# Performance work log

Hardware: AMD Instinct MI355X
Metric: run time of the kernel (lower is better)

The kernel has to match this reference:

```python
import jax, jax.numpy as jnp
import numpy as np

N_HEADS = 32
N_KV = 8
N_REP = N_HEADS // N_KV  # 4
HD = 128
ROPE_THETA = 500000.0


def _rope_tables(seq_len, hd, theta):
    inv = 1.0 / (theta ** (np.arange(0, hd, 2, dtype=np.float32) / hd))  # [hd/2]
    t = np.arange(seq_len, dtype=np.float32)
    ang = np.outer(t, inv)  # [T, hd/2]
    return jnp.asarray(np.cos(ang)), jnp.asarray(np.sin(ang))


def setup_inputs() -> dict:
    key = jax.random.key(0)
    ks = jax.random.split(key, 8)
    B, T, D = 2, 2048, 4096
    s = 0.02
    x = jax.random.normal(ks[0], (B, T, D), jnp.float32)
    wq = jax.random.normal(ks[1], (D, D), jnp.float32) * s
    wk = jax.random.normal(ks[2], (N_KV * HD, D), jnp.float32) * s
    wv = jax.random.normal(ks[3], (N_KV * HD, D), jnp.float32) * s
    wo = jax.random.normal(ks[4], (D, D), jnp.float32) * s
    cache_k = jnp.zeros((B, T, N_KV, HD), jnp.float32)
    cache_v = jnp.zeros((B, T, N_KV, HD), jnp.float32)
    cos, sin = _rope_tables(T, HD, ROPE_THETA)
    mask = jnp.zeros((1,), jnp.float32)  # accepted by forward but never applied
    return {"x": x, "wq": wq, "wk": wk, "wv": wv, "wo": wo,
            "cache_k": cache_k, "cache_v": cache_v,
            "cos": cos, "sin": sin, "mask": mask, "start_pos": 0}


def _apply_rope(t, cos, sin):
    # t: [B, T, H, HD]; pairs (t0,t1) along last dim act as complex numbers
    tr = t.reshape(*t.shape[:-1], HD // 2, 2)
    re, im = tr[..., 0], tr[..., 1]
    c = cos[None, :, None, :]  # [1,T,1,HD/2]
    s = sin[None, :, None, :]
    out = jnp.stack([re * c - im * s, re * s + im * c], axis=-1)
    return out.reshape(t.shape)


def reference(x, wq, wk, wv, wo, cache_k, cache_v, cos, sin, mask, start_pos):
    B, T, D = x.shape
    q = (x @ wq.T).reshape(B, T, N_HEADS, HD)
    k = (x @ wk.T).reshape(B, T, N_KV, HD)
    v = (x @ wv.T).reshape(B, T, N_KV, HD)

    q = _apply_rope(q, cos, sin)
    k = _apply_rope(k, cos, sin)

    # KV-cache write (start_pos is a python int)
    cache_k = cache_k.at[:, start_pos:start_pos + T].set(k)
    cache_v = cache_v.at[:, start_pos:start_pos + T].set(v)
    keys = cache_k[:, :start_pos + T]   # [B,S,Kv,HD]
    vals = cache_v[:, :start_pos + T]

    # GQA attention without materializing repeat_kv: q head h uses kv head h // N_REP
    q5 = q.reshape(B, T, N_KV, N_REP, HD)
    scale = 1.0 / jnp.sqrt(jnp.float32(HD))
    scores = jnp.einsum('btkrd,bskd->bkrts', q5, keys) * scale  # [B,Kv,Rep,T,S]
    # NOTE: source forward never adds `mask` to scores; faithfully omitted.
    probs = jax.nn.softmax(scores, axis=-1)
    ctx = jnp.einsum('bkrts,bskd->btkrd', probs, vals)  # [B,T,Kv,Rep,HD]
    cat = ctx.reshape(B, T, N_HEADS * HD)
    return cat @ wo.T
```

## Files before the change

kernel.cpp:

```cpp
#include <hip/hip_runtime.h>
#include <hip/hip_bf16.h>
#include <stdint.h>


typedef short bf16x8 __attribute__((ext_vector_type(8)));
typedef float f32x4  __attribute__((ext_vector_type(4)));

#define GLB_AS(p) ((__attribute__((address_space(1))) void*)(p))
#define LDS_AS(p) ((__attribute__((address_space(3))) void*)(p))

__device__ __forceinline__ float bf2f(ushort u) {
    union { unsigned int i; float f; } v; v.i = ((unsigned int)u) << 16; return v.f;
}
__device__ __forceinline__ ushort f2bf(float f) {
    union { float f; unsigned int i; } v; v.f = f;
    unsigned int r = v.i + 0x7FFFu + ((v.i >> 16) & 1u);
    return (ushort)(r >> 16);
}
__device__ __forceinline__ unsigned int pk_bf16(float a, float b) {
    return (unsigned int)f2bf(a) | ((unsigned int)f2bf(b) << 16);
}
__device__ __forceinline__ unsigned int cvtpk2(float lo, float hi) {
    unsigned int r;
    asm("v_cvt_pk_bf16_f32 %0, %1, %2" : "=v"(r) : "v"(lo), "v"(hi));
    return r;
}
__device__ __forceinline__ void store_c(ushort* p, float v) { *p = f2bf(v); }
__device__ __forceinline__ void store_c(float*  p, float v) { *p = v; }

__global__ __launch_bounds__(256) void cast_f2b(
    const float4* __restrict__ src, ushort4* __restrict__ dst, int n4)
{
    int i = blockIdx.x * 256 + threadIdx.x;
    if (i < n4) {
        float4 v = src[i];
        ushort4 o;
        o.x = f2bf(v.x); o.y = f2bf(v.y); o.z = f2bf(v.z); o.w = f2bf(v.w);
        dst[i] = o;
    }
}

template <typename OT>
__global__ __launch_bounds__(256) void gemm_nt(
    const ushort* __restrict__ A, const ushort* __restrict__ B,
    OT* __restrict__ C, int M, int N, int K)
{
    __shared__ __align__(16) ushort lA[128 * 32];
    __shared__ __align__(16) ushort lB[128 * 32];

    const int tid  = threadIdx.x;
    const int lane = tid & 63;
    const int w    = tid >> 6;
    const int wm   = w >> 1, wn = w & 1;
    const int quad = lane >> 4, l16 = lane & 15;
    const int bm   = blockIdx.y * 128, bn = blockIdx.x * 128;

    f32x4 acc[4][4];
#pragma unroll
    for (int i = 0; i < 4; i++)
#pragma unroll
        for (int j = 0; j < 4; j++) acc[i][j] = (f32x4){0.f, 0.f, 0.f, 0.f};

    const ushort* pa0 = A + (size_t)(bm + (tid >> 2)) * K + (tid & 3) * 8;
    const ushort* pb0 = B + (size_t)(bn + (tid >> 2)) * K + (tid & 3) * 8;
    char* ldsA0 = (char*)lA + (tid & 192) * 16;
    char* ldsA1 = ldsA0 + 4096;
    char* ldsB0 = (char*)lB + (tid & 192) * 16;
    char* ldsB1 = ldsB0 + 4096;
    const size_t rowskip = (size_t)64 * K;

    for (int k0 = 0; k0 < K; k0 += 32) {
        __builtin_amdgcn_global_load_lds(GLB_AS(pa0 + k0),           LDS_AS(ldsA0), 16, 0, 0);
        __builtin_amdgcn_global_load_lds(GLB_AS(pa0 + rowskip + k0), LDS_AS(ldsA1), 16, 0, 0);
        __builtin_amdgcn_global_load_lds(GLB_AS(pb0 + k0),           LDS_AS(ldsB0), 16, 0, 0);
        __builtin_amdgcn_global_load_lds(GLB_AS(pb0 + rowskip + k0), LDS_AS(ldsB1), 16, 0, 0);
        __syncthreads();

        bf16x8 a[4], b[4];
#pragma unroll
        for (int i = 0; i < 4; i++)
            a[i] = *(const bf16x8*)&lA[(wm * 64 + i * 16 + l16) * 32 + quad * 8];
#pragma unroll
        for (int j = 0; j < 4; j++)
            b[j] = *(const bf16x8*)&lB[(wn * 64 + j * 16 + l16) * 32 + quad * 8];
#pragma unroll
        for (int i = 0; i < 4; i++)
#pragma unroll
            for (int j = 0; j < 4; j++)
                acc[i][j] = __builtin_amdgcn_mfma_f32_16x16x32_bf16(a[i], b[j], acc[i][j], 0, 0, 0);
        __syncthreads();
    }

#pragma unroll
    for (int i = 0; i < 4; i++)
#pragma unroll
        for (int j = 0; j < 4; j++)
#pragma unroll
            for (int r = 0; r < 4; r++) {
                int row = bm + wm * 64 + i * 16 + quad * 4 + r;
                int col = bn + wn * 64 + j * 16 + l16;
                store_c(&C[(size_t)row * N + col], acc[i][j][r]);
            }
}

__global__ __launch_bounds__(256) void rope_kernel(
    ushort* __restrict__ X, const float* __restrict__ cosv,
    const float* __restrict__ sinv, int ldx, int tprs, float scale)
{
    int gid = blockIdx.x * 256 + threadIdx.x;
    int m  = gid >> tprs;
    int pi = (gid & ((1 << tprs) - 1)) * 4;
    int t  = m & 2047;
    int i  = pi & 63;
    float4 c4 = *(const float4*)&cosv[t * 64 + i];
    float4 s4 = *(const float4*)&sinv[t * 64 + i];
    ushort* px = X + (size_t)m * ldx + pi * 2;
    uint4 d = *(const uint4*)px;
    unsigned int parts[4] = {d.x, d.y, d.z, d.w};
    float cc[4] = {c4.x, c4.y, c4.z, c4.w};
    float ss[4] = {s4.x, s4.y, s4.z, s4.w};
#pragma unroll
    for (int p = 0; p < 4; p++) {
        float re = bf2f((ushort)(parts[p] & 0xffffu));
        float im = bf2f((ushort)(parts[p] >> 16));
        float re2 = (re * cc[p] - im * ss[p]) * scale;
        float im2 = (re * ss[p] + im * cc[p]) * scale;
        parts[p] = pk_bf16(re2, im2);
    }
    *(uint4*)px = make_uint4(parts[0], parts[1], parts[2], parts[3]);
}

__global__ __launch_bounds__(256) void transpose_v(
    const ushort* __restrict__ KV, ushort* __restrict__ Vt)
{
    __shared__ ushort tile[32][33];
    int n0 = blockIdx.x * 32, m0 = blockIdx.y * 32;
    int tx = threadIdx.x & 31, ty = threadIdx.x >> 5;
#pragma unroll
    for (int r = ty; r < 32; r += 8)
        tile[r][tx] = KV[(size_t)(m0 + r) * 2048 + 1024 + n0 + tx];
    __syncthreads();
    int b  = m0 >> 11;
    int t0 = m0 & 2047;
#pragma unroll
    for (int r = ty; r < 32; r += 8)
        Vt[(size_t)b * 2097152 + (size_t)(n0 + r) * 2048 + t0 + tx] = tile[tx][r];
}

__global__ __launch_bounds__(512) void flash_attn(
    const ushort* __restrict__ Q, const ushort* __restrict__ KV,
    const ushort* __restrict__ Vt, ushort* __restrict__ ctx)
{
    __shared__ __align__(16) ushort lK[64 * 128];
    __shared__ __align__(16) ushort lV[128 * 64];
    __shared__ __align__(16) ushort lP[8 * 16 * 72];

    const int qt = blockIdx.x, h = blockIdx.y, b = blockIdx.z;
    const int kv = h >> 2;
    const int tid = threadIdx.x, lane = tid & 63, w = tid >> 6;
    const int quad = lane >> 4, l16 = lane & 15;

    const int q0 = qt * 128 + w * 16;
    const size_t qrow = (size_t)(b * 2048 + q0 + l16) * 4096 + h * 128;
    bf16x8 bQ[4];
#pragma unroll
    for (int ks = 0; ks < 4; ks++)
        bQ[ks] = *(const bf16x8*)&Q[qrow + ks * 32 + quad * 8];

    f32x4 o[8];
#pragma unroll
    for (int dc = 0; dc < 8; dc++) o[dc] = (f32x4){0.f, 0.f, 0.f, 0.f};
    float m = -1e30f, l = 0.f;

    const ushort* gK = KV + (size_t)(b * 2048) * 2048 + kv * 128;
    const ushort* gV = Vt + (size_t)(b * 8 + kv) * 2048 * 128;
    ushort* pw = &lP[w * 16 * 72];

    const int keyb = tid >> 4, dsub = tid & 15;
    const int db   = tid >> 3, ssub = tid & 7;
    const ushort* baseK = gK + (size_t)keyb * 2048 + (dsub ^ (keyb & 15)) * 8;
    const ushort* baseV = gV + (size_t)db * 2048 + (ssub ^ (db & 7)) * 8;
    char* ldsK = (char*)lK + (tid & 448) * 16;
    char* ldsV = (char*)lV + (tid & 448) * 16;

    for (int s0 = 0; s0 < 2048; s0 += 64) {
#pragma unroll
        for (int rep = 0; rep < 2; rep++) {
            __builtin_amdgcn_global_load_lds(
                GLB_AS(baseK + (size_t)(s0 + rep * 32) * 2048),
                LDS_AS(ldsK + rep * 8192), 16, 0, 0);
            __builtin_amdgcn_global_load_lds(
                GLB_AS(baseV + (size_t)rep * 131072 + s0),
                LDS_AS(ldsV + rep * 8192), 16, 0, 0);
        }
        __syncthreads();

        f32x4 scT[4];
#pragma unroll
        for (int g = 0; g < 4; g++) scT[g] = (f32x4){0.f, 0.f, 0.f, 0.f};
#pragma unroll
        for (int g = 0; g < 4; g++)
#pragma unroll
            for (int ks = 0; ks < 4; ks++) {
                bf16x8 aK = *(const bf16x8*)&lK[(g * 16 + l16) * 128 + ((ks * 4 + quad) ^ l16) * 8];
                scT[g] = __builtin_amdgcn_mfma_f32_16x16x32_bf16(aK, bQ[ks], scT[g], 0, 0, 0);
            }

        float tmax = scT[0][0];
#pragma unroll
        for (int g = 0; g < 4; g++)
#pragma unroll
            for (int r = 0; r < 4; r++) tmax = fmaxf(tmax, scT[g][r]);
        tmax = fmaxf(tmax, __shfl_xor(tmax, 16, 64));
        tmax = fmaxf(tmax, __shfl_xor(tmax, 32, 64));

        if (__any(tmax > m + 8.f)) {
            float mnew = fmaxf(m, tmax);
            float alpha = exp2f(m - mnew);
            m = mnew;
            l *= alpha;
#pragma unroll
            for (int dc = 0; dc < 8; dc++)
#pragma unroll
                for (int r = 0; r < 4; r++) o[dc][r] *= alpha;
        }

        float p[16];
        float ts = 0.f;
#pragma unroll
        for (int i = 0; i < 16; i++) {
            p[i] = exp2f(scT[i >> 2][i & 3] - m);
            ts += p[i];
        }
        ts += __shfl_xor(ts, 16, 64);
        ts += __shfl_xor(ts, 32, 64);
        l += ts;

#pragma unroll
        for (int g = 0; g < 4; g++) {
            uint2 pk;
            pk.x = cvtpk2(p[g * 4 + 0], p[g * 4 + 1]);
            pk.y = cvtpk2(p[g * 4 + 2], p[g * 4 + 3]);
            *(uint2*)&pw[l16 * 72 + g * 16 + quad * 4] = pk;
        }
        bf16x8 bP[2];
#pragma unroll
        for (int c = 0; c < 2; c++)
            bP[c] = *(const bf16x8*)&pw[l16 * 72 + c * 32 + quad * 8];

#pragma unroll
        for (int dc = 0; dc < 8; dc++)
#pragma unroll
            for (int c = 0; c < 2; c++) {
                bf16x8 aV = *(const bf16x8*)&lV[(dc * 16 + l16) * 64 + ((c * 4 + quad) ^ (l16 & 7)) * 8];
                o[dc] = __builtin_amdgcn_mfma_f32_16x16x32_bf16(aV, bP[c], o[dc], 0, 0, 0);
            }
        __syncthreads();
    }

    float inv = 1.0f / l;
#pragma unroll
    for (int dc = 0; dc < 8; dc++) {
        uint2 pk;
        pk.x = cvtpk2(o[dc][0] * inv, o[dc][1] * inv);
        pk.y = cvtpk2(o[dc][2] * inv, o[dc][3] * inv);
        *(uint2*)&ctx[qrow + dc * 16 + quad * 4] = pk;
    }
}

extern "C" void kernel_launch(void* const* d_in, const int* in_sizes, int n_in,
                              void* d_out, int out_size, void* d_ws, size_t ws_size,
                              hipStream_t stream)
{
    const float* x    = (const float*)d_in[0];
    const float* wq   = (const float*)d_in[1];
    const float* wk   = (const float*)d_in[2];
    const float* wv   = (const float*)d_in[3];
    const float* wo   = (const float*)d_in[4];
    const float* cosv = (const float*)d_in[7];
    const float* sinv = (const float*)d_in[8];
    float* out = (float*)d_out;

    ushort* Xb   = (ushort*)d_ws;
    ushort* ctx  = Xb;
    ushort* Wbig = Xb   + (size_t)16 * 1024 * 1024;
    ushort* Wsm  = Wbig + (size_t)16 * 1024 * 1024;
    ushort* Vt   = Wsm;
    ushort* Q    = Wsm  + (size_t)8  * 1024 * 1024;
    ushort* KV   = Q    + (size_t)16 * 1024 * 1024;

    dim3 blk(256);
    cast_f2b<<<16384, blk, 0, stream>>>((const float4*)x,  (ushort4*)Xb,   4194304);
    cast_f2b<<<16384, blk, 0, stream>>>((const float4*)wq, (ushort4*)Wbig, 4194304);
    cast_f2b<<<4096,  blk, 0, stream>>>((const float4*)wk, (ushort4*)Wsm,  1048576);
    cast_f2b<<<4096,  blk, 0, stream>>>((const float4*)wv, (ushort4*)(Wsm + (size_t)4194304), 1048576);

    gemm_nt<<<dim3(32, 32), blk, 0, stream>>>(Xb, Wbig, Q,  4096, 4096, 4096);
    gemm_nt<<<dim3(16, 32), blk, 0, stream>>>(Xb, Wsm,  KV, 4096, 2048, 4096);

    cast_f2b<<<16384, blk, 0, stream>>>((const float4*)wo, (ushort4*)Wbig, 4194304);

    rope_kernel<<<8192, blk, 0, stream>>>(Q,  cosv, sinv, 4096, 9,
                                          0.08838834764831845f * 1.4426950408889634f);
    rope_kernel<<<2048, blk, 0, stream>>>(KV, cosv, sinv, 2048, 7, 1.0f);
    transpose_v<<<dim3(32, 128), blk, 0, stream>>>(KV, Vt);

    flash_attn<<<dim3(16, 32, 2), dim3(512), 0, stream>>>(Q, KV, Vt, ctx);

    gemm_nt<<<dim3(32, 32), blk, 0, stream>>>(ctx, Wbig, out, 4096, 4096, 4096);
}
```

Baseline: 963.4 us.

## Replace 128x128 GEMM with 256x256 double-buffered swizzled 8-wave GEMM

```diff
diff --git a/kernel.cpp b/kernel.cpp
--- a/kernel.cpp
+++ b/kernel.cpp
@@ -27,6 +27,12 @@
 }
 __device__ __forceinline__ void store_c(ushort* p, float v) { *p = f2bf(v); }
 __device__ __forceinline__ void store_c(float*  p, float v) { *p = v; }
+
+__device__ __forceinline__ void barr() {
+    asm volatile("" ::: "memory");
+    __builtin_amdgcn_s_barrier();
+    asm volatile("" ::: "memory");
+}
 
 __global__ __launch_bounds__(256) void cast_f2b(
     const float4* __restrict__ src, ushort4* __restrict__ dst, int n4)
@@ -40,67 +46,154 @@
     }
 }
 
+enum { OFF_A0 = 0, OFF_A1 = 16384, OFF_B0 = 32768, OFF_B1 = 49152, BUFSZ = 65536 };
+
+__device__ __forceinline__ void rdA(const char* half, bf16x8 (&a)[4][2],
+                                    int wm, int quad, int l16) {
+    const int cx = l16 & 7;
+#pragma unroll
+    for (int m2 = 0; m2 < 4; m2++)
+#pragma unroll
+        for (int ks = 0; ks < 2; ks++)
+            a[m2][ks] = *(const bf16x8*)(half + (wm * 64 + m2 * 16 + l16) * 128
+                                              + (((ks * 4 + quad) ^ cx) * 16));
+}
+__device__ __forceinline__ void rdB(const char* half, bf16x8 (&b)[2][2],
+                                    int wn, int quad, int l16) {
+    const int cx = l16 & 7;
+#pragma unroll
+    for (int n2 = 0; n2 < 2; n2++)
+#pragma unroll
+        for (int ks = 0; ks < 2; ks++)
+            b[n2][ks] = *(const bf16x8*)(half + (wn * 32 + n2 * 16 + l16) * 128
+                                              + (((ks * 4 + quad) ^ cx) * 16));
+}
+template <int MH, int NH>
+__device__ __forceinline__ void mmq(f32x4 (&acc)[2][2][4][2],
+                                    const bf16x8 (&a)[4][2], const bf16x8 (&b)[2][2]) {
+    __builtin_amdgcn_s_setprio(1);
+#pragma unroll
+    for (int m2 = 0; m2 < 4; m2++)
+#pragma unroll
+        for (int n2 = 0; n2 < 2; n2++)
+#pragma unroll
+            for (int ks = 0; ks < 2; ks++)
+                acc[MH][NH][m2][n2] = __builtin_amdgcn_mfma_f32_16x16x32_bf16(
+                    a[m2][ks], b[n2][ks], acc[MH][NH][m2][n2], 0, 0, 0);
+    __builtin_amdgcn_s_setprio(0);
+}
+__device__ __forceinline__ void stage_half(const char* src, char* dst, size_t kb) {
+    __builtin_amdgcn_global_load_lds(GLB_AS(src),           LDS_AS(dst),        16, 0, 0);
+    __builtin_amdgcn_global_load_lds(GLB_AS(src + 64 * kb), LDS_AS(dst + 8192), 16, 0, 0);
+}
+
+#define GATE8 asm volatile("s_waitcnt vmcnt(8)" ::: "memory")
+#define GATE0 asm volatile("s_waitcnt vmcnt(0)" ::: "memory")
+#define GATEN ((void)0)
+
+#define DO_TILE(LBUF, KO, DO_STAGE, GATE)                                        \
+    {                                                                            \
+        const char* Lb = lds + (LBUF) * BUFSZ;                                   \
+        char* Sb = ldsW + (LBUF) * BUFSZ;                                        \
+                                                         \
+        rdA(Lb + OFF_A0, a, wm, quad, l16);                                      \
+        rdB(Lb + OFF_B0, b0, wn, quad, l16);                                     \
+        barr();                                                                  \
+        mmq<0, 0>(acc, a, b0);                                                   \
+        barr();                                                                  \
+                                       \
+        rdB(Lb + OFF_B1, b1, wn, quad, l16);                                     \
+        if (DO_STAGE) {                                                          \
+            stage_half(aSrc + (KO), Sb + OFF_A0, kb);                            \
+            stage_half(bSrc + (KO), Sb + OFF_B0, kb);                            \
+        }                                                                        \
+        barr();                                                                  \
+        mmq<0, 1>(acc, a, b1);                                                   \
+        barr();                                                                  \
+                      \
+        rdA(Lb + OFF_A1, a, wm, quad, l16);                                      \
+        if (DO_STAGE) stage_half(bSrc + 128 * kb + (KO), Sb + OFF_B1, kb);       \
+        barr();                                                                  \
+        mmq<1, 1>(acc, a, b1);                                                   \
+        barr();                                                                  \
+                             \
+        if (DO_STAGE) stage_half(aSrc + 128 * kb + (KO), Sb + OFF_A1, kb);       \
+        barr();                                                                  \
+        mmq<1, 0>(acc, a, b0);                                                   \
+        GATE;                                                                    \
+        barr();                                                                  \
+    }
+
 template <typename OT>
-__global__ __launch_bounds__(256) void gemm_nt(
+__global__ __launch_bounds__(512, 2) void gemm_nt256(
     const ushort* __restrict__ A, const ushort* __restrict__ B,
-    OT* __restrict__ C, int M, int N, int K)
-{
-    __shared__ __align__(16) ushort lA[128 * 32];
-    __shared__ __align__(16) ushort lB[128 * 32];
-
-    const int tid  = threadIdx.x;
-    const int lane = tid & 63;
-    const int w    = tid >> 6;
-    const int wm   = w >> 1, wn = w & 1;
+    OT* __restrict__ C, int N, int K)
+{
+    __shared__ __align__(16) char lds[131072];
+
+    const int tid = threadIdx.x, lane = tid & 63, w = tid >> 6;
+    const int wm = w >> 2, wn = w & 3;
     const int quad = lane >> 4, l16 = lane & 15;
-    const int bm   = blockIdx.y * 128, bn = blockIdx.x * 128;
-
-    f32x4 acc[4][4];
-#pragma unroll
-    for (int i = 0; i < 4; i++)
-#pragma unroll
-        for (int j = 0; j < 4; j++) acc[i][j] = (f32x4){0.f, 0.f, 0.f, 0.f};
-
-    const ushort* pa0 = A + (size_t)(bm + (tid >> 2)) * K + (tid & 3) * 8;
-    const ushort* pb0 = B + (size_t)(bn + (tid >> 2)) * K + (tid & 3) * 8;
-    char* ldsA0 = (char*)lA + (tid & 192) * 16;
-    char* ldsA1 = ldsA0 + 4096;
-    char* ldsB0 = (char*)lB + (tid & 192) * 16;
-    char* ldsB1 = ldsB0 + 4096;
-    const size_t rowskip = (size_t)64 * K;
-
-    for (int k0 = 0; k0 < K; k0 += 32) {
-        __builtin_amdgcn_global_load_lds(GLB_AS(pa0 + k0),           LDS_AS(ldsA0), 16, 0, 0);
-        __builtin_amdgcn_global_load_lds(GLB_AS(pa0 + rowskip + k0), LDS_AS(ldsA1), 16, 0, 0);
-        __builtin_amdgcn_global_load_lds(GLB_AS(pb0 + k0),           LDS_AS(ldsB0), 16, 0, 0);
-        __builtin_amdgcn_global_load_lds(GLB_AS(pb0 + rowskip + k0), LDS_AS(ldsB1), 16, 0, 0);
-        __syncthreads();
-
-        bf16x8 a[4], b[4];
-#pragma unroll
-        for (int i = 0; i < 4; i++)
-            a[i] = *(const bf16x8*)&lA[(wm * 64 + i * 16 + l16) * 32 + quad * 8];
-#pragma unroll
-        for (int j = 0; j < 4; j++)
-            b[j] = *(const bf16x8*)&lB[(wn * 64 + j * 16 + l16) * 32 + quad * 8];
-#pragma unroll
-        for (int i = 0; i < 4; i++)
-#pragma unroll
-            for (int j = 0; j < 4; j++)
-                acc[i][j] = __builtin_amdgcn_mfma_f32_16x16x32_bf16(a[i], b[j], acc[i][j], 0, 0, 0);
-        __syncthreads();
-    }
-
-#pragma unroll
-    for (int i = 0; i < 4; i++)
-#pragma unroll
-        for (int j = 0; j < 4; j++)
-#pragma unroll
-            for (int r = 0; r < 4; r++) {
-                int row = bm + wm * 64 + i * 16 + quad * 4 + r;
-                int col = bn + wn * 64 + j * 16 + l16;
-                store_c(&C[(size_t)row * N + col], acc[i][j][r]);
-            }
+
+    const int nwg = gridDim.x;
+    const int swz = ((int)blockIdx.x & 7) * (nwg >> 3) + ((int)blockIdx.x >> 3);
+    const int nx  = N >> 8;
+    const int bm  = (swz / nx) * 256, bn = (swz % nx) * 256;
+
+    const size_t kb = (size_t)K * 2;
+
+    const int srow = tid >> 3;
+    const int gch  = (tid & 7) ^ (srow & 7);
+    const char* aSrc = (const char*)A + (size_t)(bm + srow) * kb + gch * 16;
+    const char* bSrc = (const char*)B + (size_t)(bn + srow) * kb + gch * 16;
+    char* ldsW = lds + w * 1024;
+
+    f32x4 acc[2][2][4][2];
+#pragma unroll
+    for (int i = 0; i < 2; i++)
+#pragma unroll
+        for (int j = 0; j < 2; j++)
+#pragma unroll
+            for (int m2 = 0; m2 < 4; m2++)
+#pragma unroll
+                for (int n2 = 0; n2 < 2; n2++)
+                    acc[i][j][m2][n2] = (f32x4){0.f, 0.f, 0.f, 0.f};
+
+    bf16x8 a[4][2], b0[2][2], b1[2][2];
+
+    stage_half(aSrc,                ldsW + OFF_A0, kb);
+    stage_half(aSrc + 128 * kb,     ldsW + OFF_A1, kb);
+    stage_half(bSrc,                ldsW + OFF_B0, kb);
+    stage_half(bSrc + 128 * kb,     ldsW + OFF_B1, kb);
+    stage_half(aSrc + 128,            ldsW + BUFSZ + OFF_A0, kb);
+    stage_half(aSrc + 128 * kb + 128, ldsW + BUFSZ + OFF_A1, kb);
+    stage_half(bSrc + 128,            ldsW + BUFSZ + OFF_B0, kb);
+    stage_half(bSrc + 128 * kb + 128, ldsW + BUFSZ + OFF_B1, kb);
+    GATE8;
+    barr();
+
+    int ko = 256;
+    for (int it = 0; it < 31; ++it, ko += 256) {
+        DO_TILE(0, ko,       true, GATE8);
+        DO_TILE(1, ko + 128, true, GATE8);
+    }
+    DO_TILE(0, 0, false, GATE0);
+    DO_TILE(1, 0, false, GATEN);
+
+#pragma unroll
+    for (int MH = 0; MH < 2; MH++)
+#pragma unroll
+        for (int NH = 0; NH < 2; NH++)
+#pragma unroll
+            for (int m2 = 0; m2 < 4; m2++)
+#pragma unroll
+                for (int n2 = 0; n2 < 2; n2++)
+#pragma unroll
+                    for (int r = 0; r < 4; r++) {
+                        int row = bm + MH * 128 + wm * 64 + m2 * 16 + quad * 4 + r;
+                        int col = bn + NH * 128 + wn * 32 + n2 * 16 + l16;
+                        store_c(&C[(size_t)row * N + col], acc[MH][NH][m2][n2][r]);
+                    }
 }
 
 __global__ __launch_bounds__(256) void rope_kernel(
@@ -295,8 +388,8 @@
     cast_f2b<<<4096,  blk, 0, stream>>>((const float4*)wk, (ushort4*)Wsm,  1048576);
     cast_f2b<<<4096,  blk, 0, stream>>>((const float4*)wv, (ushort4*)(Wsm + (size_t)4194304), 1048576);
 
-    gemm_nt<<<dim3(32, 32), blk, 0, stream>>>(Xb, Wbig, Q,  4096, 4096, 4096);
-    gemm_nt<<<dim3(16, 32), blk, 0, stream>>>(Xb, Wsm,  KV, 4096, 2048, 4096);
+    gemm_nt256<<<dim3(256), dim3(512), 0, stream>>>(Xb, Wbig, Q,  4096, 4096);
+    gemm_nt256<<<dim3(128), dim3(512), 0, stream>>>(Xb, Wsm,  KV, 2048, 4096);
 
     cast_f2b<<<16384, blk, 0, stream>>>((const float4*)wo, (ushort4*)Wbig, 4194304);
 
@@ -307,5 +400,5 @@
 
     flash_attn<<<dim3(16, 32, 2), dim3(512), 0, stream>>>(Q, KV, Vt, ctx);
 
-    gemm_nt<<<dim3(32, 32), blk, 0, stream>>>(ctx, Wbig, out, 4096, 4096, 4096);
-}
+    gemm_nt256<<<dim3(256), dim3(512), 0, stream>>>(ctx, Wbig, out, 4096, 4096);
+}
```

Result: faster. 771.8 us (-19.9%).
